# Kernel optimization log

Hardware: AMD Instinct MI355X
Metric: run time of the kernel (lower is better)

Reference implementation:

```python
import jax, jax.numpy as jnp
import numpy as np

B, N, H = 2, 2048, 8
HID = 16


def setup_inputs() -> dict:
    key = jax.random.key(0)
    ks = jax.random.split(key, 11)
    def lin(k, fan_in, fan_out):
        bound = 1.0 / np.sqrt(fan_in)
        kw, kb = jax.random.split(k)
        W = jax.random.uniform(kw, (fan_in, fan_out), jnp.float32, -bound, bound)
        b = jax.random.uniform(kb, (fan_out,), jnp.float32, -bound, bound)
        return W, b
    xyz = jax.random.normal(ks[0], (B, N, 3), jnp.float32)
    Wd1, bd1 = lin(ks[1], 1, HID)
    Wd2, bd2 = lin(ks[2], HID, H)
    Wr1, br1 = lin(ks[3], 3, HID)
    Wr2, br2 = lin(ks[4], HID, H)
    Wf, bf = lin(ks[5], 2 * H, H)
    return {"xyz": xyz, "Wd1": Wd1, "bd1": bd1, "Wd2": Wd2, "bd2": bd2,
            "Wr1": Wr1, "br1": br1, "Wr2": Wr2, "br2": br2, "Wf": Wf, "bf": bf}


def reference(xyz, Wd1, bd1, Wd2, bd2, Wr1, br1, Wr2, br2, Wf, bf):
    # xyz: [B, N, 3].  rel_pos[b,i,j] = xyz[b,j] - xyz[b,i]  (unsqueeze(1) - unsqueeze(2))
    rel = xyz[:, None, :, :] - xyz[:, :, None, :]          # [B, N, N, 3]
    dist = jnp.sqrt(jnp.sum(rel * rel, axis=-1, keepdims=True))  # [B, N, N, 1]
    # distance encoder: Linear(1,16) -> ReLU -> Linear(16,H)
    d_bias = jax.nn.relu(dist @ Wd1 + bd1) @ Wd2 + bd2     # [B, N, N, H]
    # direction encoder: normalized direction -> Linear(3,16) -> ReLU -> Linear(16,H)
    direction = rel / (dist + 1e-7)
    r_bias = jax.nn.relu(direction @ Wr1 + br1) @ Wr2 + br2  # [B, N, N, H]
    # fusion overwrites the additive bias in the original module
    fused = jnp.concatenate([d_bias, r_bias], axis=-1) @ Wf + bf  # [B, N, N, H]
    return jnp.transpose(fused, (0, 3, 1, 2))              # [B, H, N, N]
```

## Files before the change

### kernel.cpp

```cpp
#include <hip/hip_runtime.h>


#define BB 2
#define NN 2048
#define HH 8

typedef _Float16 f16x8 __attribute__((ext_vector_type(8)));
typedef float    f32x16 __attribute__((ext_vector_type(16)));

__global__ __launch_bounds__(256) void erpe_fold_weights(
    const float* __restrict__ Wd2, const float* __restrict__ bd2,
    const float* __restrict__ Wr2, const float* __restrict__ br2,
    const float* __restrict__ Wf,  const float* __restrict__ bf,
    float* __restrict__ ws)
{
    int t = threadIdx.x;
    if (t < 128) {
        int k = t >> 3, h = t & 7;
        float sa = 0.f, sb = 0.f;
        #pragma unroll
        for (int m = 0; m < HH; ++m) {
            sa += Wd2[k * HH + m] * Wf[m * HH + h];
            sb += Wr2[k * HH + m] * Wf[(m + HH) * HH + h];
        }
        ws[t]       = sa;
        ws[128 + t] = sb;
    } else if (t < 136) {
        int h = t - 128;
        float s = bf[h];
        #pragma unroll
        for (int m = 0; m < HH; ++m)
            s += bd2[m] * Wf[m * HH + h] + br2[m] * Wf[(m + HH) * HH + h];
        ws[256 + h] = s;
    }
}

__global__ __launch_bounds__(256) void erpe_main(
    const float* __restrict__ xyz,
    const float* __restrict__ Wd1, const float* __restrict__ bd1,
    const float* __restrict__ Wr1, const float* __restrict__ br1,
    const float* __restrict__ ws,
    float* __restrict__ out)
{
    const int tid  = threadIdx.x;
    const int wave = tid >> 6;
    const int lane = tid & 63;
    const int g    = lane >> 5;
    const int jl   = lane & 31;

    const int blk = blockIdx.x;
    const int i   = blk & (NN - 1);
    const int b   = blk >> 11;

    const int kb = g * 8;
    float wd[8], bdv[8], w0[8], w1[8], w2[8], brv[8];
    #pragma unroll
    for (int e = 0; e < 8; ++e) {
        wd[e]  = Wd1[kb + e];
        bdv[e] = bd1[kb + e];
        w0[e]  = Wr1[0 * 16 + kb + e];
        w1[e]  = Wr1[1 * 16 + kb + e];
        w2[e]  = Wr1[2 * 16 + kb + e];
        brv[e] = br1[kb + e];
    }

    f16x8 A1, A2;
    #pragma unroll
    for (int e = 0; e < 8; ++e) {
        if (jl < 8) {
            A1[e] = (_Float16)ws[(kb + e) * 8 + jl];
            A2[e] = (_Float16)ws[128 + (kb + e) * 8 + jl];
        } else {
            A1[e] = (_Float16)0.f;
            A2[e] = (_Float16)0.f;
        }
    }
    float cb[4];
    #pragma unroll
    for (int r = 0; r < 4; ++r) cb[r] = ws[256 + g * 4 + r];

    const float* xb = xyz + (size_t)b * NN * 3;
    const float xi = xb[i * 3 + 0];
    const float yi = xb[i * 3 + 1];
    const float zi = xb[i * 3 + 2];

    float* ob = out + ((size_t)b * HH) * (size_t)NN * NN + (size_t)i * NN;
    const int jwave = wave * 512;

    for (int t2 = 0; t2 < 8; ++t2) {
        const int jg = jwave + t2 * 64;

        #pragma unroll
        for (int p = 0; p < 2; ++p) {
            const int j = jg + p * 32 + jl;
            const float ax = xb[j * 3 + 0];
            const float ay = xb[j * 3 + 1];
            const float az = xb[j * 3 + 2];
            const float dx = ax - xi, dy = ay - yi, dz = az - zi;
            const float r2 = fmaf(dx, dx, fmaf(dy, dy, dz * dz));
            const float d  = __builtin_amdgcn_sqrtf(r2);
            const float inv = __builtin_amdgcn_rcpf(d + 1e-7f);
            const float ux = dx * inv, uy = dy * inv, uz = dz * inv;

            f16x8 Btd, Btr;
            #pragma unroll
            for (int e = 0; e < 8; ++e) {
                const float td = fmaxf(fmaf(d, wd[e], bdv[e]), 0.f);
                const float tr = fmaxf(
                    fmaf(ux, w0[e], fmaf(uy, w1[e], fmaf(uz, w2[e], brv[e]))),
                    0.f);
                Btd[e] = (_Float16)td;
                Btr[e] = (_Float16)tr;
            }

            f32x16 acc;
            #pragma unroll
            for (int q = 0; q < 16; ++q) acc[q] = (q < 4) ? cb[q] : 0.f;
            acc = __builtin_amdgcn_mfma_f32_32x32x16_f16(A1, Btd, acc, 0, 0, 0);
            acc = __builtin_amdgcn_mfma_f32_32x32x16_f16(A2, Btr, acc, 0, 0, 0);

            #pragma unroll
            for (int r = 0; r < 4; ++r)
                ob[(size_t)(r + 4 * g) * NN * NN + j] = acc[r];
        }
    }
}

extern "C" void kernel_launch(void* const* d_in, const int* in_sizes, int n_in,
                              void* d_out, int out_size, void* d_ws, size_t ws_size,
                              hipStream_t stream) {
    const float* xyz = (const float*)d_in[0];
    const float* Wd1 = (const float*)d_in[1];
    const float* bd1 = (const float*)d_in[2];
    const float* Wd2 = (const float*)d_in[3];
    const float* bd2 = (const float*)d_in[4];
    const float* Wr1 = (const float*)d_in[5];
    const float* br1 = (const float*)d_in[6];
    const float* Wr2 = (const float*)d_in[7];
    const float* br2 = (const float*)d_in[8];
    const float* Wf  = (const float*)d_in[9];
    const float* bf  = (const float*)d_in[10];
    float* out = (float*)d_out;
    float* ws  = (float*)d_ws;

    erpe_fold_weights<<<1, 256, 0, stream>>>(Wd2, bd2, Wr2, br2, Wf, bf, ws);
    erpe_main<<<BB * NN, 256, 0, stream>>>(xyz, Wd1, bd1, Wr1, br1, ws, out);
}
```

Baseline: 57.97 us.

## Fold weights inside main kernel and compute hidden layer in packed fp16

Removes the separate weight-folding launch: every block now computes the folded Wd2·Wf, Wr2·Wf and bias products itself from the raw weights. The first-layer activations are computed with packed half2 arithmetic (pk_fma/pk_max) instead of per-element fp32 FMAs plus conversions. The j loop is flattened and output pointer arithmetic simplified. This trades a kernel launch and some VALU work for redundant per-block weight folding and reduced fp16 precision in the hidden layer.

```diff
diff --git a/kernel.cpp b/kernel.cpp
--- a/kernel.cpp
+++ b/kernel.cpp
@@ -5,41 +5,23 @@
 #define NN 2048
 #define HH 8
 
-typedef _Float16 f16x8 __attribute__((ext_vector_type(8)));
+typedef _Float16 f16x2  __attribute__((ext_vector_type(2)));
+typedef _Float16 f16x8  __attribute__((ext_vector_type(8)));
 typedef float    f32x16 __attribute__((ext_vector_type(16)));
 
-__global__ __launch_bounds__(256) void erpe_fold_weights(
-    const float* __restrict__ Wd2, const float* __restrict__ bd2,
-    const float* __restrict__ Wr2, const float* __restrict__ br2,
-    const float* __restrict__ Wf,  const float* __restrict__ bf,
-    float* __restrict__ ws)
-{
-    int t = threadIdx.x;
-    if (t < 128) {
-        int k = t >> 3, h = t & 7;
-        float sa = 0.f, sb = 0.f;
-        #pragma unroll
-        for (int m = 0; m < HH; ++m) {
-            sa += Wd2[k * HH + m] * Wf[m * HH + h];
-            sb += Wr2[k * HH + m] * Wf[(m + HH) * HH + h];
-        }
-        ws[t]       = sa;
-        ws[128 + t] = sb;
-    } else if (t < 136) {
-        int h = t - 128;
-        float s = bf[h];
-        #pragma unroll
-        for (int m = 0; m < HH; ++m)
-            s += bd2[m] * Wf[m * HH + h] + br2[m] * Wf[(m + HH) * HH + h];
-        ws[256 + h] = s;
-    }
+union B8 { f16x2 p[4]; f16x8 v; };
+
+static __device__ __forceinline__ f16x2 pkrtz(float a, float b) {
+    return __builtin_bit_cast(f16x2, __builtin_amdgcn_cvt_pkrtz(a, b));
 }
 
 __global__ __launch_bounds__(256) void erpe_main(
     const float* __restrict__ xyz,
     const float* __restrict__ Wd1, const float* __restrict__ bd1,
+    const float* __restrict__ Wd2, const float* __restrict__ bd2,
     const float* __restrict__ Wr1, const float* __restrict__ br1,
-    const float* __restrict__ ws,
+    const float* __restrict__ Wr2, const float* __restrict__ br2,
+    const float* __restrict__ Wf,  const float* __restrict__ bf,
     float* __restrict__ out)
 {
     const int tid  = threadIdx.x;
@@ -53,76 +35,88 @@
     const int b   = blk >> 11;
 
     const int kb = g * 8;
-    float wd[8], bdv[8], w0[8], w1[8], w2[8], brv[8];
+    f16x2 wdp[4], bdp[4], w0p[4], w1p[4], w2p[4], brp[4];
     #pragma unroll
-    for (int e = 0; e < 8; ++e) {
-        wd[e]  = Wd1[kb + e];
-        bdv[e] = bd1[kb + e];
-        w0[e]  = Wr1[0 * 16 + kb + e];
-        w1[e]  = Wr1[1 * 16 + kb + e];
-        w2[e]  = Wr1[2 * 16 + kb + e];
-        brv[e] = br1[kb + e];
+    for (int p = 0; p < 4; ++p) {
+        const int k0 = kb + 2 * p;
+        wdp[p][0] = (_Float16)Wd1[k0];     wdp[p][1] = (_Float16)Wd1[k0 + 1];
+        bdp[p][0] = (_Float16)bd1[k0];     bdp[p][1] = (_Float16)bd1[k0 + 1];
+        w0p[p][0] = (_Float16)Wr1[k0];     w0p[p][1] = (_Float16)Wr1[k0 + 1];
+        w1p[p][0] = (_Float16)Wr1[16+k0];  w1p[p][1] = (_Float16)Wr1[16+k0+1];
+        w2p[p][0] = (_Float16)Wr1[32+k0];  w2p[p][1] = (_Float16)Wr1[32+k0+1];
+        brp[p][0] = (_Float16)br1[k0];     brp[p][1] = (_Float16)br1[k0 + 1];
     }
 
+    const int hA = jl & 7;
     f16x8 A1, A2;
     #pragma unroll
     for (int e = 0; e < 8; ++e) {
-        if (jl < 8) {
-            A1[e] = (_Float16)ws[(kb + e) * 8 + jl];
-            A2[e] = (_Float16)ws[128 + (kb + e) * 8 + jl];
-        } else {
-            A1[e] = (_Float16)0.f;
-            A2[e] = (_Float16)0.f;
+        float sa = 0.f, sb = 0.f;
+        #pragma unroll
+        for (int m = 0; m < 8; ++m) {
+            sa = fmaf(Wd2[(kb + e) * 8 + m], Wf[m * 8 + hA], sa);
+            sb = fmaf(Wr2[(kb + e) * 8 + m], Wf[(m + 8) * 8 + hA], sb);
         }
+        A1[e] = (jl < 8) ? (_Float16)sa : (_Float16)0.f;
+        A2[e] = (jl < 8) ? (_Float16)sb : (_Float16)0.f;
     }
-    float cb[4];
+
+    f32x16 accInit;
     #pragma unroll
-    for (int r = 0; r < 4; ++r) cb[r] = ws[256 + g * 4 + r];
+    for (int q = 0; q < 16; ++q) accInit[q] = 0.f;
+    #pragma unroll
+    for (int r = 0; r < 4; ++r) {
+        const int h = g * 4 + r;
+        float s = bf[h];
+        #pragma unroll
+        for (int m = 0; m < 8; ++m)
+            s = fmaf(bd2[m], Wf[m * 8 + h],
+                fmaf(br2[m], Wf[(m + 8) * 8 + h], s));
+        accInit[r] = s;
+    }
 
     const float* xb = xyz + (size_t)b * NN * 3;
     const float xi = xb[i * 3 + 0];
     const float yi = xb[i * 3 + 1];
     const float zi = xb[i * 3 + 2];
 
-    float* ob = out + ((size_t)b * HH) * (size_t)NN * NN + (size_t)i * NN;
-    const int jwave = wave * 512;
+    float* op = out + ((size_t)b * HH + 4 * g) * (size_t)NN * NN
+                    + (size_t)i * NN + wave * 512 + jl;
 
-    for (int t2 = 0; t2 < 8; ++t2) {
-        const int jg = jwave + t2 * 64;
+    const f16x2 z2 = { (_Float16)0.f, (_Float16)0.f };
+
+    for (int t2 = 0; t2 < 16; ++t2) {
+        const int j = wave * 512 + t2 * 32 + jl;
+        const float ax = xb[j * 3 + 0];
+        const float ay = xb[j * 3 + 1];
+        const float az = xb[j * 3 + 2];
+        const float dx = ax - xi, dy = ay - yi, dz = az - zi;
+        const float r2 = fmaf(dx, dx, fmaf(dy, dy, dz * dz));
+        const float d  = __builtin_amdgcn_sqrtf(r2);
+        const float inv = __builtin_amdgcn_rcpf(d + 1e-7f);
+        const float ux = dx * inv, uy = dy * inv, uz = dz * inv;
+
+        const f16x2 d2  = pkrtz(d, d);
+        const f16x2 ux2 = pkrtz(ux, ux);
+        const f16x2 uy2 = pkrtz(uy, uy);
+        const f16x2 uz2 = pkrtz(uz, uz);
+
+        B8 Btd, Btr;
+        #pragma unroll
+        for (int p = 0; p < 4; ++p) {
+            f16x2 td = d2 * wdp[p] + bdp[p];
+            f16x2 tr = ux2 * w0p[p] + (uy2 * w1p[p] + (uz2 * w2p[p] + brp[p]));
+            Btd.p[p] = __builtin_elementwise_max(td, z2);
+            Btr.p[p] = __builtin_elementwise_max(tr, z2);
+        }
+
+        f32x16 acc;
+        acc = __builtin_amdgcn_mfma_f32_32x32x16_f16(A1, Btd.v, accInit, 0, 0, 0);
+        acc = __builtin_amdgcn_mfma_f32_32x32x16_f16(A2, Btr.v, acc,     0, 0, 0);
 
         #pragma unroll
-        for (int p = 0; p < 2; ++p) {
-            const int j = jg + p * 32 + jl;
-            const float ax = xb[j * 3 + 0];
-            const float ay = xb[j * 3 + 1];
-            const float az = xb[j * 3 + 2];
-            const float dx = ax - xi, dy = ay - yi, dz = az - zi;
-            const float r2 = fmaf(dx, dx, fmaf(dy, dy, dz * dz));
-            const float d  = __builtin_amdgcn_sqrtf(r2);
-            const float inv = __builtin_amdgcn_rcpf(d + 1e-7f);
-            const float ux = dx * inv, uy = dy * inv, uz = dz * inv;
-
-            f16x8 Btd, Btr;
-            #pragma unroll
-            for (int e = 0; e < 8; ++e) {
-                const float td = fmaxf(fmaf(d, wd[e], bdv[e]), 0.f);
-                const float tr = fmaxf(
-                    fmaf(ux, w0[e], fmaf(uy, w1[e], fmaf(uz, w2[e], brv[e]))),
-                    0.f);
-                Btd[e] = (_Float16)td;
-                Btr[e] = (_Float16)tr;
-            }
-
-            f32x16 acc;
-            #pragma unroll
-            for (int q = 0; q < 16; ++q) acc[q] = (q < 4) ? cb[q] : 0.f;
-            acc = __builtin_amdgcn_mfma_f32_32x32x16_f16(A1, Btd, acc, 0, 0, 0);
-            acc = __builtin_amdgcn_mfma_f32_32x32x16_f16(A2, Btr, acc, 0, 0, 0);
-
-            #pragma unroll
-            for (int r = 0; r < 4; ++r)
-                ob[(size_t)(r + 4 * g) * NN * NN + j] = acc[r];
-        }
+        for (int r = 0; r < 4; ++r)
+            op[(size_t)r * NN * NN + t2 * 32] = acc[r];
     }
 }
 
@@ -141,8 +135,7 @@
     const float* Wf  = (const float*)d_in[9];
     const float* bf  = (const float*)d_in[10];
     float* out = (float*)d_out;
-    float* ws  = (float*)d_ws;
 
-    erpe_fold_weights<<<1, 256, 0, stream>>>(Wd2, bd2, Wr2, br2, Wf, bf, ws);
-    erpe_main<<<BB * NN, 256, 0, stream>>>(xyz, Wd1, bd1, Wr1, br1, ws, out);
+    erpe_main<<<BB * NN, 256, 0, stream>>>(xyz, Wd1, bd1, Wd2, bd2,
+                                           Wr1, br1, Wr2, br2, Wf, bf, out);
 }
```

Result: slower. 66.67 us (+15.0%).
